# Kernel tuning notes

Measured on AMD Instinct MI355X. Metric: run time of the kernel, lower is better.

Reference implementation:

```python
import jax, jax.numpy as jnp
import numpy as np

B, S, D = 4, 2048, 1024
E, H = 1024, 16
HD = E // H
TEMPERATURE = 1.0


def setup_inputs() -> dict:
    key = jax.random.key(0)
    ks = jax.random.split(key, 6)
    x = jax.random.normal(ks[0], (B, S, D), dtype=jnp.float32)
    src_key_padding_mask = jnp.zeros((B, S), dtype=bool)  # unused by module
    matrix_mask = jax.random.normal(ks[1], (B, S, S), dtype=jnp.float32)
    # Xavier-uniform linear weights (torch Linear stores [out, in])
    lim_qkv = float(np.sqrt(6.0 / (D + 3 * E)))
    qkv_w = jax.random.uniform(ks[2], (3 * E, D), dtype=jnp.float32, minval=-lim_qkv, maxval=lim_qkv)
    qkv_b = jnp.zeros((3 * E,), dtype=jnp.float32)
    lim_o = float(np.sqrt(6.0 / (E + E)))
    o_w = jax.random.uniform(ks[3], (E, E), dtype=jnp.float32, minval=-lim_o, maxval=lim_o)
    o_b = jnp.zeros((E,), dtype=jnp.float32)
    return {"x": x, "src_key_padding_mask": src_key_padding_mask, "matrix_mask": matrix_mask,
            "qkv_w": qkv_w, "qkv_b": qkv_b, "o_w": o_w, "o_b": o_b}


def reference(x, src_key_padding_mask, matrix_mask, qkv_w, qkv_b, o_w, o_b):
    b, s, _ = x.shape
    qkv = x @ qkv_w.T + qkv_b                      # [B,S,3E]
    qkv = qkv.reshape(b, s, H, 3 * HD).transpose(0, 2, 1, 3)  # [B,H,S,3*HD]
    q, k, v = jnp.split(qkv, 3, axis=-1)           # each [B,H,S,HD]
    scale = 1.0 / np.sqrt(HD)
    logits = jnp.einsum('bhqd,bhkd->bhqk', q, k) * scale + matrix_mask[:, None, :, :]
    attn = jax.nn.softmax(logits / TEMPERATURE, axis=-1)  # [B,H,S,S]
    # dropout=0.0, eval mode -> no-op
    values = jnp.einsum('bhqk,bhkd->bhqd', attn, v)       # [B,H,S,HD]
    values = values.transpose(0, 2, 1, 3).reshape(b, s, E)
    o = values @ o_w.T + o_b                       # [B,S,E]
    attention_mean = jnp.mean(attn, axis=1)        # [B,S,S]
    return (o, attention_mean)
```

## Files before the change

### kernel.cpp

```cpp
#include <hip/hip_runtime.h>

#define B_ 4
#define S_ 2048
#define D_ 1024
#define E_ 1024
#define H_ 16
#define HD_ 64
#define SCALE 0.125f
#define LOG2E 1.44269504f
#define C1_ (SCALE * LOG2E)

typedef __bf16 bf16;
typedef __bf16 bf16x8 __attribute__((ext_vector_type(8)));
typedef __bf16 bf16x4 __attribute__((ext_vector_type(4)));
typedef float f32x4 __attribute__((ext_vector_type(4)));
typedef _Float16 f16x8 __attribute__((ext_vector_type(8)));
typedef _Float16 f16x4 __attribute__((ext_vector_type(4)));

static __device__ __forceinline__ f32x4 mfma16(bf16x8 a, bf16x8 b, f32x4 c) {
  return __builtin_amdgcn_mfma_f32_16x16x32_bf16(a, b, c, 0, 0, 0);
}

typedef __attribute__((address_space(3))) void lvoid;
typedef const __attribute__((address_space(1))) void gvoid;
static __device__ __forceinline__ void gload16(const void* g, void* l) {
  __builtin_amdgcn_global_load_lds((gvoid*)g, (lvoid*)l, 16, 0, 0);
}

static __device__ __forceinline__ float exp2a(float x) {
  float r;
  asm("v_exp_f32 %0, %1" : "=v"(r) : "v"(x));
  return r;
}

static __device__ __forceinline__ int rsw(int row) {
  return (row & 3) | (((row >> 3) & 1) << 2);
}

__global__ __launch_bounds__(256) void k_cvtall(const float* __restrict__ x, bf16* __restrict__ xb,
                                                const float* __restrict__ qkvw, bf16* __restrict__ wb,
                                                const float* __restrict__ ow, bf16* __restrict__ owb,
                                                const float* __restrict__ msk, _Float16* __restrict__ bm) {
  int bid = blockIdx.x;
  const float* src;
  int i;
  if (bid < 8192) {
    i = bid * 256 + threadIdx.x;
    float4 v = reinterpret_cast<const float4*>(x)[i];
    bf16x4 o = { (bf16)v.x, (bf16)v.y, (bf16)v.z, (bf16)v.w };
    reinterpret_cast<bf16x4*>(xb)[i] = o;
  } else if (bid < 11264) {
    i = (bid - 8192) * 256 + threadIdx.x;
    float4 v = reinterpret_cast<const float4*>(qkvw)[i];
    bf16x4 o = { (bf16)v.x, (bf16)v.y, (bf16)v.z, (bf16)v.w };
    reinterpret_cast<bf16x4*>(wb)[i] = o;
  } else if (bid < 12288) {
    i = (bid - 11264) * 256 + threadIdx.x;
    float4 v = reinterpret_cast<const float4*>(ow)[i];
    bf16x4 o = { (bf16)v.x, (bf16)v.y, (bf16)v.z, (bf16)v.w };
    reinterpret_cast<bf16x4*>(owb)[i] = o;
  } else {
    i = (bid - 12288) * 256 + threadIdx.x;
    float4 v = reinterpret_cast<const float4*>(msk)[i];
    f16x4 o = { (_Float16)(v.x * LOG2E), (_Float16)(v.y * LOG2E),
                (_Float16)(v.z * LOG2E), (_Float16)(v.w * LOG2E) };
    reinterpret_cast<f16x4*>(bm)[i] = o;
  }
  (void)src;
}

__global__ __launch_bounds__(256) void k_qkv(const bf16* __restrict__ xb,
                                             const bf16* __restrict__ wb,
                                             const float* __restrict__ qkvb,
                                             bf16* __restrict__ Qw,
                                             bf16* __restrict__ Kw,
                                             bf16* __restrict__ Vtw) {
  __shared__ __align__(16) bf16 lA[128 * 32];
  __shared__ __align__(16) bf16 lB[128 * 32];
  const int tid = threadIdx.x, lane = tid & 63, wv = tid >> 6;
  const int u = lane >> 4, c = lane & 15;
  const int wr = wv >> 1, wc = wv & 1;
  const int m0 = blockIdx.y * 128;
  const int n0 = blockIdx.x * 128;
  const int sr = tid >> 2, sk = (tid & 3) * 8;
  const bf16* gA = xb + (size_t)(m0 + sr) * D_ + sk;
  const bf16* gB = wb + (size_t)(n0 + sr) * D_ + sk;
  bf16* lpA = lA + wv * 512;
  bf16* lpB = lB + wv * 512;
  f32x4 acc[4][4] = {};
  for (int k0 = 0; k0 < D_; k0 += 32) {
    gload16(gA + k0, lpA);
    gload16(gA + 64 * D_ + k0, lpA + 2048);
    gload16(gB + k0, lpB);
    gload16(gB + 64 * D_ + k0, lpB + 2048);
    __syncthreads();
    bf16x8 af[4], bfr[4];
#pragma unroll
    for (int m = 0; m < 4; ++m)
      af[m] = *(const bf16x8*)(lA + (wr * 64 + m * 16 + c) * 32 + u * 8);
#pragma unroll
    for (int n = 0; n < 4; ++n)
      bfr[n] = *(const bf16x8*)(lB + (wc * 64 + n * 16 + c) * 32 + u * 8);
#pragma unroll
    for (int m = 0; m < 4; ++m)
#pragma unroll
      for (int n = 0; n < 4; ++n)
        acc[m][n] = mfma16(af[m], bfr[n], acc[m][n]);
    __syncthreads();
  }
#pragma unroll
  for (int n = 0; n < 4; ++n) {
    int nn = n0 + wc * 64 + n * 16 + c;
    float bias = qkvb[nn];
    int h = nn / 192;
    int rem = nn - h * 192;
#pragma unroll
    for (int m = 0; m < 4; ++m) {
#pragma unroll
      for (int r = 0; r < 4; ++r) {
        int q = m0 + wr * 64 + m * 16 + 4 * u + r;
        int bb = q >> 11, s = q & 2047;
        bf16 v = (bf16)(acc[m][n][r] + bias);
        if (rem < 64)       Qw[((bb * H_ + h) * S_ + s) * HD_ + rem] = v;
        else if (rem < 128) Kw[((bb * H_ + h) * S_ + s) * HD_ + (rem - 64)] = v;
        else                Vtw[((bb * H_ + h) * HD_ + (rem - 128)) * S_ + s] = v;
      }
    }
  }
}

#define PV_TILE2(HC, HN, BS, KT, PF)                                          \
  {                                                                           \
    f32x4 sA[4], sB[4];                                                       \
    _Pragma("unroll")                                                         \
    for (int f = 0; f < 4; ++f) {                                             \
      int rk = 32 * (f & 1) + 8 * (c >> 2) + 4 * (f >> 1) + (c & 3);          \
      int sw = rsw(rk);                                                       \
      bf16x8 k0 = *(const bf16x8*)&kl[BS][rk * 64 + ((u ^ sw) * 8)];          \
      bf16x8 k1 = *(const bf16x8*)&kl[BS][rk * 64 + (((4 + u) ^ sw) * 8)];    \
      f32x4 a = {};                                                           \
      a = mfma16(k0, aqA0, a);                                                \
      a = mfma16(k1, aqA1, a);                                                \
      sA[f] = a;                                                              \
      f32x4 bb2 = {};                                                         \
      bb2 = mfma16(k0, aqB0, bb2);                                            \
      bb2 = mfma16(k1, aqB1, bb2);                                            \
      sB[f] = bb2;                                                            \
    }                                                                         \
    if (PF) {                                                                 \
      const bf16* ksrc = Kb + (size_t)((KT) + 1) * 64 * HD_;                  \
      gload16(ksrc + ksw1, (bf16*)kl[(BS) ^ 1] + wv * 512);                   \
      gload16(ksrc + ksw2, (bf16*)kl[(BS) ^ 1] + 2048 + wv * 512);            \
      const bf16* vsrc = Vb + (size_t)((KT) + 1) * 64;                        \
      gload16(vsrc + vsw1, (bf16*)vl[(BS) ^ 1] + wv * 512);                   \
      gload16(vsrc + vsw2, (bf16*)vl[(BS) ^ 1] + 2048 + wv * 512);            \
      const _Float16* nA = bmrA + ((KT) + 1) * 64 + 8 * u;                    \
      const _Float16* nB = bmrB + ((KT) + 1) * 64 + 8 * u;                    \
      HN[0] = *(const f16x8*)(nA);                                            \
      HN[1] = *(const f16x8*)(nA + 32);                                       \
      HN[2] = *(const f16x8*)(nB);                                            \
      HN[3] = *(const f16x8*)(nB + 32);                                       \
    }                                                                         \
    float pA[16], pB[16];                                                     \
    _Pragma("unroll")                                                         \
    for (int f = 0; f < 4; ++f) {                                             \
      _Pragma("unroll")                                                       \
      for (int j = 0; j < 4; ++j) {                                           \
        float p = exp2a(sA[f][j] * C1_ + (float)HC[f & 1][4 * (f >> 1) + j]); \
        lsumA += p;                                                           \
        pA[f * 4 + j] = p;                                                    \
        float q2 = exp2a(sB[f][j] * C1_ +                                     \
                         (float)HC[2 + (f & 1)][4 * (f >> 1) + j]);           \
        lsumB += q2;                                                          \
        pB[f * 4 + j] = q2;                                                   \
      }                                                                       \
    }                                                                         \
    bf16x8 bpA0 = { (bf16)pA[0],  (bf16)pA[1],  (bf16)pA[2],  (bf16)pA[3],    \
                    (bf16)pA[8],  (bf16)pA[9],  (bf16)pA[10], (bf16)pA[11] }; \
    bf16x8 bpA1 = { (bf16)pA[4],  (bf16)pA[5],  (bf16)pA[6],  (bf16)pA[7],    \
                    (bf16)pA[12], (bf16)pA[13], (bf16)pA[14], (bf16)pA[15] }; \
    bf16x8 bpB0 = { (bf16)pB[0],  (bf16)pB[1],  (bf16)pB[2],  (bf16)pB[3],    \
                    (bf16)pB[8],  (bf16)pB[9],  (bf16)pB[10], (bf16)pB[11] }; \
    bf16x8 bpB1 = { (bf16)pB[4],  (bf16)pB[5],  (bf16)pB[6],  (bf16)pB[7],    \
                    (bf16)pB[12], (bf16)pB[13], (bf16)pB[14], (bf16)pB[15] }; \
    __builtin_amdgcn_s_setprio(1);                                            \
    _Pragma("unroll")                                                         \
    for (int g = 0; g < 4; ++g) {                                             \
      int rv = g * 16 + c;                                                    \
      int swv = rsw(rv);                                                      \
      bf16x8 v0 = *(const bf16x8*)&vl[BS][rv * 64 + ((u ^ swv) * 8)];         \
      bf16x8 v1 = *(const bf16x8*)&vl[BS][rv * 64 + (((4 + u) ^ swv) * 8)];   \
      accA[g] = mfma16(v0, bpA0, accA[g]);                                    \
      accA[g] = mfma16(v1, bpA1, accA[g]);                                    \
      accB[g] = mfma16(v0, bpB0, accB[g]);                                    \
      accB[g] = mfma16(v1, bpB1, accB[g]);                                    \
    }                                                                         \
    __builtin_amdgcn_s_setprio(0);                                            \
    __syncthreads();                                                          \
  }

__global__ __launch_bounds__(256) void k_pv(const bf16* __restrict__ Qw,
                                            const bf16* __restrict__ Kw,
                                            const bf16* __restrict__ Vtw,
                                            const _Float16* __restrict__ bmask,
                                            float* __restrict__ li_ws,
                                            bf16* __restrict__ valw) {
  __shared__ __align__(16) bf16 kl[2][64 * 64];
  __shared__ __align__(16) bf16 vl[2][64 * 64];
  const int tid = threadIdx.x, lane = tid & 63, wv = tid >> 6;
  const int u = lane >> 4, c = lane & 15;
  const int qt = blockIdx.x, h = blockIdx.y, b = blockIdx.z;
  const bf16* Qb = Qw + (size_t)(b * H_ + h) * S_ * HD_;
  const bf16* Kb = Kw + (size_t)(b * H_ + h) * S_ * HD_;
  const bf16* Vb = Vtw + (size_t)(b * H_ + h) * HD_ * S_;
  const int qrA = qt * 128 + wv * 32 + c;
  const int qrB = qrA + 16;
  bf16x8 aqA0 = *(const bf16x8*)(Qb + (size_t)qrA * HD_ + u * 8);
  bf16x8 aqA1 = *(const bf16x8*)(Qb + (size_t)qrA * HD_ + 32 + u * 8);
  bf16x8 aqB0 = *(const bf16x8*)(Qb + (size_t)qrB * HD_ + u * 8);
  bf16x8 aqB1 = *(const bf16x8*)(Qb + (size_t)qrB * HD_ + 32 + u * 8);
  const _Float16* bmrA = bmask + (size_t)b * S_ * S_ + (size_t)qrA * S_;
  const _Float16* bmrB = bmask + (size_t)b * S_ * S_ + (size_t)qrB * S_;
  const int r1 = tid >> 3, s1 = (tid & 7) ^ rsw(tid >> 3);
  const int g2i = tid + 256;
  const int r2 = g2i >> 3, s2 = (g2i & 7) ^ rsw(g2i >> 3);
  const int ksw1 = (r1 * 8 + s1) * 8, ksw2 = (r2 * 8 + s2) * 8;
  const int vsw1 = r1 * S_ + s1 * 8, vsw2 = r2 * S_ + s2 * 8;
  gload16(Kb + ksw1, (bf16*)kl[0] + wv * 512);
  gload16(Kb + ksw2, (bf16*)kl[0] + 2048 + wv * 512);
  gload16(Vb + vsw1, (bf16*)vl[0] + wv * 512);
  gload16(Vb + vsw2, (bf16*)vl[0] + 2048 + wv * 512);
  f16x8 hmA[4], hmB[4];
  hmA[0] = *(const f16x8*)(bmrA + 8 * u);
  hmA[1] = *(const f16x8*)(bmrA + 32 + 8 * u);
  hmA[2] = *(const f16x8*)(bmrB + 8 * u);
  hmA[3] = *(const f16x8*)(bmrB + 32 + 8 * u);
  f32x4 accA[4] = {}, accB[4] = {};
  float lsumA = 0.f, lsumB = 0.f;
  __syncthreads();
  for (int kt2 = 0; kt2 < 16; ++kt2) {
    PV_TILE2(hmA, hmB, 0, 2 * kt2, true);
    PV_TILE2(hmB, hmA, 1, 2 * kt2 + 1, (kt2 < 15));
  }
  lsumA += __shfl_xor(lsumA, 16, 64);
  lsumA += __shfl_xor(lsumA, 32, 64);
  lsumB += __shfl_xor(lsumB, 16, 64);
  lsumB += __shfl_xor(lsumB, 32, 64);
  float liA = 1.f / lsumA, liB = 1.f / lsumB;
  if (u == 0) {
    li_ws[(b * H_ + h) * S_ + qrA] = liA;
    li_ws[(b * H_ + h) * S_ + qrB] = liB;
  }
#pragma unroll
  for (int g = 0; g < 4; ++g) {
    bf16x4 pkA = { (bf16)(accA[g][0] * liA), (bf16)(accA[g][1] * liA),
                   (bf16)(accA[g][2] * liA), (bf16)(accA[g][3] * liA) };
    *(bf16x4*)(&valw[(size_t)(b * S_ + qrA) * E_ + h * HD_ + g * 16 + 4 * u]) = pkA;
    bf16x4 pkB = { (bf16)(accB[g][0] * liB), (bf16)(accB[g][1] * liB),
                   (bf16)(accB[g][2] * liB), (bf16)(accB[g][3] * liB) };
    *(bf16x4*)(&valw[(size_t)(b * S_ + qrB) * E_ + h * HD_ + g * 16 + 4 * u]) = pkB;
  }
}

#define MEAN_PHASE(QC0, QC1, QC2, QC3, QN0, QN1, QN2, QN3, BS, HH, PF)         \
  {                                                                            \
    if (PF) {                                                                  \
      const bf16* ksrc = Kw + (size_t)(bh0 + (HH) + 1) * S_ * HD_ +            \
                         (size_t)kt * 64 * HD_;                                \
      gload16(ksrc + sw1, (bf16*)kl2[(BS) ^ 1] + wv * 512);                    \
      gload16(ksrc + sw2, (bf16*)kl2[(BS) ^ 1] + 2048 + wv * 512);             \
      __builtin_amdgcn_sched_barrier(0);                                       \
    }                                                                          \
    bf16x8 kf[8];                                                              \
    _Pragma("unroll")                                                          \
    for (int f = 0; f < 4; ++f) {                                              \
      int row = f * 16 + c;                                                    \
      int sw = row & 7;                                                        \
      kf[2 * f]     = *(const bf16x8*)&kl2[BS][row * 64 + ((u ^ sw) * 8)];     \
      kf[2 * f + 1] = *(const bf16x8*)&kl2[BS][row * 64 + (((4 + u) ^ sw) * 8)];\
    }                                                                          \
    if (PF) {                                                                  \
      const bf16* Qn = Qw + (size_t)(bh0 + (HH) + 1) * S_ * HD_ +              \
                       (size_t)(qrow0 + c) * HD_ + u * 8;                      \
      QN0 = *(const bf16x8*)(Qn);                                              \
      QN1 = *(const bf16x8*)(Qn + 32);                                         \
      QN2 = *(const bf16x8*)(Qn + 64 * HD_);                                   \
      QN3 = *(const bf16x8*)(Qn + 64 * HD_ + 32);                              \
    }                                                                          \
    float llA = li_l[(HH) * 128 + wv * 16 + c];                                \
    float llB = li_l[(HH) * 128 + 64 + wv * 16 + c];                           \
    _Pragma("unroll")                                                          \
    for (int f = 0; f < 4; ++f) {                                              \
      f32x4 a = {};                                                            \
      a = mfma16(kf[2 * f], QC0, a);                                           \
      a = mfma16(kf[2 * f + 1], QC1, a);                                       \
      f32x4 bb = {};                                                           \
      bb = mfma16(kf[2 * f], QC2, bb);                                         \
      bb = mfma16(kf[2 * f + 1], QC3, bb);                                     \
      _Pragma("unroll")                                                        \
      for (int j = 0; j < 4; ++j) {                                            \
        maccA[f][j] += exp2a(a[j] * C1_ + (float)mhA[f][j]) * llA;             \
        maccB[f][j] += exp2a(bb[j] * C1_ + (float)mhB[f][j]) * llB;            \
      }                                                                        \
    }                                                                          \
    asm volatile("s_waitcnt vmcnt(4) lgkmcnt(0)" ::: "memory");                \
    __builtin_amdgcn_s_barrier();                                              \
  }

__global__ __launch_bounds__(256) void k_mean(const bf16* __restrict__ Qw,
                                              const bf16* __restrict__ Kw,
                                              const _Float16* __restrict__ bmask,
                                              const float* __restrict__ li_ws,
                                              float* __restrict__ mean_out) {
  __shared__ float li_l[H_ * 128];
  __shared__ __align__(16) bf16 kl2[2][64 * 64];
  const int tid = threadIdx.x, lane = tid & 63, wv = tid >> 6;
  const int u = lane >> 4, c = lane & 15;
  const int qt = blockIdx.x, kt = blockIdx.y, b = blockIdx.z;
  const int bh0 = b * H_;
  for (int i = tid; i < H_ * 128; i += 256) {
    int hh = i >> 7, q = i & 127;
    li_l[i] = li_ws[(bh0 + hh) * S_ + qt * 128 + q];
  }
  const int qrow0 = qt * 128 + wv * 16;
  f16x4 mhA[4], mhB[4];
  {
    const _Float16* bmpA = bmask + (size_t)b * S_ * S_ +
                           (size_t)(qrow0 + c) * S_ + (size_t)kt * 64 + 4 * u;
    const _Float16* bmpB = bmpA + (size_t)64 * S_;
#pragma unroll
    for (int f = 0; f < 4; ++f) {
      mhA[f] = *(const f16x4*)(bmpA + f * 16);
      mhB[f] = *(const f16x4*)(bmpB + f * 16);
    }
  }
  const int gg1 = wv * 64 + lane;
  const int gg2 = gg1 + 256;
  const int sw1 = (gg1 ^ ((gg1 >> 3) & 7)) * 8;
  const int sw2 = (gg2 ^ ((gg2 >> 3) & 7)) * 8;
  {
    const bf16* K0 = Kw + (size_t)bh0 * S_ * HD_ + (size_t)kt * 64 * HD_;
    gload16(K0 + sw1, (bf16*)kl2[0] + wv * 512);
    gload16(K0 + sw2, (bf16*)kl2[0] + 2048 + wv * 512);
  }
  bf16x8 qA0, qA1, qA2, qA3, qB0, qB1, qB2, qB3;
  {
    const bf16* Q0 = Qw + (size_t)bh0 * S_ * HD_ + (size_t)(qrow0 + c) * HD_ + u * 8;
    qA0 = *(const bf16x8*)Q0;
    qA1 = *(const bf16x8*)(Q0 + 32);
    qA2 = *(const bf16x8*)(Q0 + 64 * HD_);
    qA3 = *(const bf16x8*)(Q0 + 64 * HD_ + 32);
  }
  f32x4 maccA[4] = {}, maccB[4] = {};
  __syncthreads();
  for (int h2 = 0; h2 < 8; ++h2) {
    MEAN_PHASE(qA0, qA1, qA2, qA3, qB0, qB1, qB2, qB3, 0, 2 * h2, true);
    MEAN_PHASE(qB0, qB1, qB2, qB3, qA0, qA1, qA2, qA3, 1, 2 * h2 + 1, (h2 < 7));
  }
#pragma unroll
  for (int f = 0; f < 4; ++f) {
    f32x4 moA = maccA[f] * (1.f / 16.f);
    *(f32x4*)&mean_out[(size_t)b * S_ * S_ + (size_t)(qrow0 + c) * S_ +
                       (size_t)kt * 64 + f * 16 + 4 * u] = moA;
    f32x4 moB = maccB[f] * (1.f / 16.f);
    *(f32x4*)&mean_out[(size_t)b * S_ * S_ + (size_t)(qrow0 + 64 + c) * S_ +
                       (size_t)kt * 64 + f * 16 + 4 * u] = moB;
  }
}

__global__ __launch_bounds__(256) void k_oproj(const bf16* __restrict__ vb,
                                               const bf16* __restrict__ wo,
                                               const float* __restrict__ ob,
                                               float* __restrict__ out) {
  __shared__ __align__(16) bf16 lA[128 * 32];
  __shared__ __align__(16) bf16 lB[128 * 32];
  const int tid = threadIdx.x, lane = tid & 63, wv = tid >> 6;
  const int u = lane >> 4, c = lane & 15;
  const int wr = wv >> 1, wc = wv & 1;
  const int m0 = blockIdx.y * 128;
  const int n0 = blockIdx.x * 128;
  const int sr = tid >> 2, sk = (tid & 3) * 8;
  const bf16* gA = vb + (size_t)(m0 + sr) * E_ + sk;
  const bf16* gB = wo + (size_t)(n0 + sr) * E_ + sk;
  bf16* lpA = lA + wv * 512;
  bf16* lpB = lB + wv * 512;
  f32x4 acc[4][4] = {};
  for (int k0 = 0; k0 < E_; k0 += 32) {
    gload16(gA + k0, lpA);
    gload16(gA + 64 * E_ + k0, lpA + 2048);
    gload16(gB + k0, lpB);
    gload16(gB + 64 * E_ + k0, lpB + 2048);
    __syncthreads();
    bf16x8 af[4], bfr[4];
#pragma unroll
    for (int m = 0; m < 4; ++m)
      af[m] = *(const bf16x8*)(lA + (wr * 64 + m * 16 + c) * 32 + u * 8);
#pragma unroll
    for (int n = 0; n < 4; ++n)
      bfr[n] = *(const bf16x8*)(lB + (wc * 64 + n * 16 + c) * 32 + u * 8);
#pragma unroll
    for (int m = 0; m < 4; ++m)
#pragma unroll
      for (int n = 0; n < 4; ++n)
        acc[m][n] = mfma16(af[m], bfr[n], acc[m][n]);
    __syncthreads();
  }
#pragma unroll
  for (int n = 0; n < 4; ++n) {
    int nn = n0 + wc * 64 + n * 16 + c;
    float bias = ob[nn];
#pragma unroll
    for (int m = 0; m < 4; ++m) {
#pragma unroll
      for (int r = 0; r < 4; ++r) {
        int q = m0 + wr * 64 + m * 16 + 4 * u + r;
        out[(size_t)q * E_ + nn] = acc[m][n][r] + bias;
      }
    }
  }
}

extern "C" void kernel_launch(void* const* d_in, const int* in_sizes, int n_in,
                              void* d_out, int out_size, void* d_ws, size_t ws_size,
                              hipStream_t stream) {
  const float* x    = (const float*)d_in[0];
  const float* mmsk = (const float*)d_in[2];
  const float* qkvw = (const float*)d_in[3];
  const float* qkvb = (const float*)d_in[4];
  const float* ow   = (const float*)d_in[5];
  const float* ob   = (const float*)d_in[6];

  char* ws = (char*)d_ws;
  bf16* xb  = (bf16*)(ws);
  bf16* wb  = (bf16*)(ws + (16u << 20));
  bf16* owb = (bf16*)(ws + (22u << 20));
  bf16* Qw  = (bf16*)(ws + (24u << 20));
  bf16* Kw  = (bf16*)(ws + (40u << 20));
  bf16* Vtw = (bf16*)(ws + (56u << 20));
  float* li_ws = (float*)(ws + (16u << 20));
  bf16* values = xb;

  float* out_o    = (float*)d_out;
  float* out_mean = out_o + (size_t)B_ * S_ * E_;
  _Float16* bmask = (_Float16*)out_o;

  k_cvtall<<<dim3(28672), 256, 0, stream>>>(x, xb, qkvw, wb, ow, owb, mmsk, bmask);
  k_qkv<<<dim3(24, 64), 256, 0, stream>>>(xb, wb, qkvb, Qw, Kw, Vtw);
  k_pv<<<dim3(16, 16, 4), 256, 0, stream>>>(Qw, Kw, Vtw, bmask, li_ws, values);
  k_mean<<<dim3(16, 32, 4), 256, 0, stream>>>(Qw, Kw, bmask, li_ws, out_mean);
  k_oproj<<<dim3(8, 64), 256, 0, stream>>>(values, owb, ob, out_o);
}
```

Before: 331.1 us.

## Merge attention-mean and output-projection kernels into one horizontally fused launch

Combines the k_mean and k_oproj kernels into a single launch of 2560 blocks: the first 2048 compute the head-averaged attention map and the remaining 512 do the output projection GEMM, sharing one 24KB shared-memory buffer. The bf16-scaled mask moves from the output buffer into workspace, because the projection now writes out_o while mean blocks may still read the mask. This removes one launch boundary and lets the GEMM tail overlap the mean work. The cost is that occupancy is bounded by the larger shared-memory and register footprint of the two paths.

```diff
diff --git a/kernel.cpp b/kernel.cpp
--- a/kernel.cpp
+++ b/kernel.cpp
@@ -42,7 +42,6 @@
                                                 const float* __restrict__ ow, bf16* __restrict__ owb,
                                                 const float* __restrict__ msk, _Float16* __restrict__ bm) {
   int bid = blockIdx.x;
-  const float* src;
   int i;
   if (bid < 8192) {
     i = bid * 256 + threadIdx.x;
@@ -66,7 +65,6 @@
                 (_Float16)(v.z * LOG2E), (_Float16)(v.w * LOG2E) };
     reinterpret_cast<f16x4*>(bm)[i] = o;
   }
-  (void)src;
 }
 
 __global__ __launch_bounds__(256) void k_qkv(const bf16* __restrict__ xb,
@@ -267,8 +265,8 @@
     if (PF) {                                                                  \
       const bf16* ksrc = Kw + (size_t)(bh0 + (HH) + 1) * S_ * HD_ +            \
                          (size_t)kt * 64 * HD_;                                \
-      gload16(ksrc + sw1, (bf16*)kl2[(BS) ^ 1] + wv * 512);                    \
-      gload16(ksrc + sw2, (bf16*)kl2[(BS) ^ 1] + 2048 + wv * 512);             \
+      gload16(ksrc + sw1, (bf16*)(kl2 + ((BS) ^ 1) * 4096) + wv * 512);        \
+      gload16(ksrc + sw2, (bf16*)(kl2 + ((BS) ^ 1) * 4096) + 2048 + wv * 512); \
       __builtin_amdgcn_sched_barrier(0);                                       \
     }                                                                          \
     bf16x8 kf[8];                                                              \
@@ -276,8 +274,8 @@
     for (int f = 0; f < 4; ++f) {                                              \
       int row = f * 16 + c;                                                    \
       int sw = row & 7;                                                        \
-      kf[2 * f]     = *(const bf16x8*)&kl2[BS][row * 64 + ((u ^ sw) * 8)];     \
-      kf[2 * f + 1] = *(const bf16x8*)&kl2[BS][row * 64 + (((4 + u) ^ sw) * 8)];\
+      kf[2 * f]     = *(const bf16x8*)&kl2[(BS) * 4096 + row * 64 + ((u ^ sw) * 8)]; \
+      kf[2 * f + 1] = *(const bf16x8*)&kl2[(BS) * 4096 + row * 64 + (((4 + u) ^ sw) * 8)]; \
     }                                                                          \
     if (PF) {                                                                  \
       const bf16* Qn = Qw + (size_t)(bh0 + (HH) + 1) * S_ * HD_ +              \
@@ -307,114 +305,116 @@
     __builtin_amdgcn_s_barrier();                                              \
   }
 
-__global__ __launch_bounds__(256) void k_mean(const bf16* __restrict__ Qw,
-                                              const bf16* __restrict__ Kw,
-                                              const _Float16* __restrict__ bmask,
-                                              const float* __restrict__ li_ws,
-                                              float* __restrict__ mean_out) {
-  __shared__ float li_l[H_ * 128];
-  __shared__ __align__(16) bf16 kl2[2][64 * 64];
+__global__ __launch_bounds__(256) void k_mo(const bf16* __restrict__ Qw,
+                                            const bf16* __restrict__ Kw,
+                                            const _Float16* __restrict__ bmask,
+                                            const float* __restrict__ li_ws,
+                                            float* __restrict__ mean_out,
+                                            const bf16* __restrict__ vb,
+                                            const bf16* __restrict__ wo,
+                                            const float* __restrict__ ob,
+                                            float* __restrict__ out) {
+  __shared__ __align__(16) char smem[24 * 1024];
   const int tid = threadIdx.x, lane = tid & 63, wv = tid >> 6;
   const int u = lane >> 4, c = lane & 15;
-  const int qt = blockIdx.x, kt = blockIdx.y, b = blockIdx.z;
-  const int bh0 = b * H_;
-  for (int i = tid; i < H_ * 128; i += 256) {
-    int hh = i >> 7, q = i & 127;
-    li_l[i] = li_ws[(bh0 + hh) * S_ + qt * 128 + q];
-  }
-  const int qrow0 = qt * 128 + wv * 16;
-  f16x4 mhA[4], mhB[4];
-  {
-    const _Float16* bmpA = bmask + (size_t)b * S_ * S_ +
-                           (size_t)(qrow0 + c) * S_ + (size_t)kt * 64 + 4 * u;
-    const _Float16* bmpB = bmpA + (size_t)64 * S_;
+  const int bid = blockIdx.x;
+  if (bid < 2048) {
+    float* li_l = (float*)smem;
+    bf16* kl2 = (bf16*)(smem + 8192);
+    const int qt = bid & 15, kt = (bid >> 4) & 31, b = bid >> 9;
+    const int bh0 = b * H_;
+    for (int i = tid; i < H_ * 128; i += 256) {
+      int hh = i >> 7, q = i & 127;
+      li_l[i] = li_ws[(bh0 + hh) * S_ + qt * 128 + q];
+    }
+    const int qrow0 = qt * 128 + wv * 16;
+    f16x4 mhA[4], mhB[4];
+    {
+      const _Float16* bmpA = bmask + (size_t)b * S_ * S_ +
+                             (size_t)(qrow0 + c) * S_ + (size_t)kt * 64 + 4 * u;
+      const _Float16* bmpB = bmpA + (size_t)64 * S_;
+#pragma unroll
+      for (int f = 0; f < 4; ++f) {
+        mhA[f] = *(const f16x4*)(bmpA + f * 16);
+        mhB[f] = *(const f16x4*)(bmpB + f * 16);
+      }
+    }
+    const int gg1 = wv * 64 + lane;
+    const int gg2 = gg1 + 256;
+    const int sw1 = (gg1 ^ ((gg1 >> 3) & 7)) * 8;
+    const int sw2 = (gg2 ^ ((gg2 >> 3) & 7)) * 8;
+    {
+      const bf16* K0 = Kw + (size_t)bh0 * S_ * HD_ + (size_t)kt * 64 * HD_;
+      gload16(K0 + sw1, kl2 + wv * 512);
+      gload16(K0 + sw2, kl2 + 2048 + wv * 512);
+    }
+    bf16x8 qA0, qA1, qA2, qA3, qB0, qB1, qB2, qB3;
+    {
+      const bf16* Q0 = Qw + (size_t)bh0 * S_ * HD_ + (size_t)(qrow0 + c) * HD_ + u * 8;
+      qA0 = *(const bf16x8*)Q0;
+      qA1 = *(const bf16x8*)(Q0 + 32);
+      qA2 = *(const bf16x8*)(Q0 + 64 * HD_);
+      qA3 = *(const bf16x8*)(Q0 + 64 * HD_ + 32);
+    }
+    f32x4 maccA[4] = {}, maccB[4] = {};
+    __syncthreads();
+    for (int h2 = 0; h2 < 8; ++h2) {
+      MEAN_PHASE(qA0, qA1, qA2, qA3, qB0, qB1, qB2, qB3, 0, 2 * h2, true);
+      MEAN_PHASE(qB0, qB1, qB2, qB3, qA0, qA1, qA2, qA3, 1, 2 * h2 + 1, (h2 < 7));
+    }
 #pragma unroll
     for (int f = 0; f < 4; ++f) {
-      mhA[f] = *(const f16x4*)(bmpA + f * 16);
-      mhB[f] = *(const f16x4*)(bmpB + f * 16);
-    }
-  }
-  const int gg1 = wv * 64 + lane;
-  const int gg2 = gg1 + 256;
-  const int sw1 = (gg1 ^ ((gg1 >> 3) & 7)) * 8;
-  const int sw2 = (gg2 ^ ((gg2 >> 3) & 7)) * 8;
-  {
-    const bf16* K0 = Kw + (size_t)bh0 * S_ * HD_ + (size_t)kt * 64 * HD_;
-    gload16(K0 + sw1, (bf16*)kl2[0] + wv * 512);
-    gload16(K0 + sw2, (bf16*)kl2[0] + 2048 + wv * 512);
-  }
-  bf16x8 qA0, qA1, qA2, qA3, qB0, qB1, qB2, qB3;
-  {
-    const bf16* Q0 = Qw + (size_t)bh0 * S_ * HD_ + (size_t)(qrow0 + c) * HD_ + u * 8;
-    qA0 = *(const bf16x8*)Q0;
-    qA1 = *(const bf16x8*)(Q0 + 32);
-    qA2 = *(const bf16x8*)(Q0 + 64 * HD_);
-    qA3 = *(const bf16x8*)(Q0 + 64 * HD_ + 32);
-  }
-  f32x4 maccA[4] = {}, maccB[4] = {};
-  __syncthreads();
-  for (int h2 = 0; h2 < 8; ++h2) {
-    MEAN_PHASE(qA0, qA1, qA2, qA3, qB0, qB1, qB2, qB3, 0, 2 * h2, true);
-    MEAN_PHASE(qB0, qB1, qB2, qB3, qA0, qA1, qA2, qA3, 1, 2 * h2 + 1, (h2 < 7));
-  }
-#pragma unroll
-  for (int f = 0; f < 4; ++f) {
-    f32x4 moA = maccA[f] * (1.f / 16.f);
-    *(f32x4*)&mean_out[(size_t)b * S_ * S_ + (size_t)(qrow0 + c) * S_ +
-                       (size_t)kt * 64 + f * 16 + 4 * u] = moA;
-    f32x4 moB = maccB[f] * (1.f / 16.f);
-    *(f32x4*)&mean_out[(size_t)b * S_ * S_ + (size_t)(qrow0 + 64 + c) * S_ +
-                       (size_t)kt * 64 + f * 16 + 4 * u] = moB;
-  }
-}
-
-__global__ __launch_bounds__(256) void k_oproj(const bf16* __restrict__ vb,
-                                               const bf16* __restrict__ wo,
-                                               const float* __restrict__ ob,
-                                               float* __restrict__ out) {
-  __shared__ __align__(16) bf16 lA[128 * 32];
-  __shared__ __align__(16) bf16 lB[128 * 32];
-  const int tid = threadIdx.x, lane = tid & 63, wv = tid >> 6;
-  const int u = lane >> 4, c = lane & 15;
-  const int wr = wv >> 1, wc = wv & 1;
-  const int m0 = blockIdx.y * 128;
-  const int n0 = blockIdx.x * 128;
-  const int sr = tid >> 2, sk = (tid & 3) * 8;
-  const bf16* gA = vb + (size_t)(m0 + sr) * E_ + sk;
-  const bf16* gB = wo + (size_t)(n0 + sr) * E_ + sk;
-  bf16* lpA = lA + wv * 512;
-  bf16* lpB = lB + wv * 512;
-  f32x4 acc[4][4] = {};
-  for (int k0 = 0; k0 < E_; k0 += 32) {
-    gload16(gA + k0, lpA);
-    gload16(gA + 64 * E_ + k0, lpA + 2048);
-    gload16(gB + k0, lpB);
-    gload16(gB + 64 * E_ + k0, lpB + 2048);
-    __syncthreads();
-    bf16x8 af[4], bfr[4];
-#pragma unroll
-    for (int m = 0; m < 4; ++m)
-      af[m] = *(const bf16x8*)(lA + (wr * 64 + m * 16 + c) * 32 + u * 8);
-#pragma unroll
-    for (int n = 0; n < 4; ++n)
-      bfr[n] = *(const bf16x8*)(lB + (wc * 64 + n * 16 + c) * 32 + u * 8);
-#pragma unroll
-    for (int m = 0; m < 4; ++m)
+      f32x4 moA = maccA[f] * (1.f / 16.f);
+      *(f32x4*)&mean_out[(size_t)b * S_ * S_ + (size_t)(qrow0 + c) * S_ +
+                         (size_t)kt * 64 + f * 16 + 4 * u] = moA;
+      f32x4 moB = maccB[f] * (1.f / 16.f);
+      *(f32x4*)&mean_out[(size_t)b * S_ * S_ + (size_t)(qrow0 + 64 + c) * S_ +
+                         (size_t)kt * 64 + f * 16 + 4 * u] = moB;
+    }
+  } else {
+    bf16* lA = (bf16*)smem;
+    bf16* lB = (bf16*)(smem + 8192);
+    const int bid2 = bid - 2048;
+    const int wr = wv >> 1, wc = wv & 1;
+    const int m0 = (bid2 >> 3) * 128;
+    const int n0 = (bid2 & 7) * 128;
+    const int sr = tid >> 2, sk = (tid & 3) * 8;
+    const bf16* gA = vb + (size_t)(m0 + sr) * E_ + sk;
+    const bf16* gB = wo + (size_t)(n0 + sr) * E_ + sk;
+    bf16* lpA = lA + wv * 512;
+    bf16* lpB = lB + wv * 512;
+    f32x4 acc[4][4] = {};
+    for (int k0 = 0; k0 < E_; k0 += 32) {
+      gload16(gA + k0, lpA);
+      gload16(gA + 64 * E_ + k0, lpA + 2048);
+      gload16(gB + k0, lpB);
+      gload16(gB + 64 * E_ + k0, lpB + 2048);
+      __syncthreads();
+      bf16x8 af[4], bfr[4];
+#pragma unroll
+      for (int m = 0; m < 4; ++m)
+        af[m] = *(const bf16x8*)(lA + (wr * 64 + m * 16 + c) * 32 + u * 8);
 #pragma unroll
       for (int n = 0; n < 4; ++n)
-        acc[m][n] = mfma16(af[m], bfr[n], acc[m][n]);
-    __syncthreads();
-  }
-#pragma unroll
-  for (int n = 0; n < 4; ++n) {
-    int nn = n0 + wc * 64 + n * 16 + c;
-    float bias = ob[nn];
-#pragma unroll
-    for (int m = 0; m < 4; ++m) {
-#pragma unroll
-      for (int r = 0; r < 4; ++r) {
-        int q = m0 + wr * 64 + m * 16 + 4 * u + r;
-        out[(size_t)q * E_ + nn] = acc[m][n][r] + bias;
+        bfr[n] = *(const bf16x8*)(lB + (wc * 64 + n * 16 + c) * 32 + u * 8);
+#pragma unroll
+      for (int m = 0; m < 4; ++m)
+#pragma unroll
+        for (int n = 0; n < 4; ++n)
+          acc[m][n] = mfma16(af[m], bfr[n], acc[m][n]);
+      __syncthreads();
+    }
+#pragma unroll
+    for (int n = 0; n < 4; ++n) {
+      int nn = n0 + wc * 64 + n * 16 + c;
+      float bias = ob[nn];
+#pragma unroll
+      for (int m = 0; m < 4; ++m) {
+#pragma unroll
+        for (int r = 0; r < 4; ++r) {
+          int q = m0 + wr * 64 + m * 16 + 4 * u + r;
+          out[(size_t)q * E_ + nn] = acc[m][n][r] + bias;
+        }
       }
     }
   }
@@ -442,11 +442,11 @@
 
   float* out_o    = (float*)d_out;
   float* out_mean = out_o + (size_t)B_ * S_ * E_;
-  _Float16* bmask = (_Float16*)out_o;
+  _Float16* bmask = (_Float16*)(ws + (72u << 20));
 
   k_cvtall<<<dim3(28672), 256, 0, stream>>>(x, xb, qkvw, wb, ow, owb, mmsk, bmask);
   k_qkv<<<dim3(24, 64), 256, 0, stream>>>(xb, wb, qkvb, Qw, Kw, Vtw);
   k_pv<<<dim3(16, 16, 4), 256, 0, stream>>>(Qw, Kw, Vtw, bmask, li_ws, values);
-  k_mean<<<dim3(16, 32, 4), 256, 0, stream>>>(Qw, Kw, bmask, li_ws, out_mean);
-  k_oproj<<<dim3(8, 64), 256, 0, stream>>>(values, owb, ob, out_o);
-}
+  k_mo<<<dim3(2560), 256, 0, stream>>>(Qw, Kw, bmask, li_ws, out_mean,
+                                       values, owb, ob, out_o);
+}
```

Result: no change. 332.3 us (+0.4%).

## Split mean kernel into single-wave blocks without barriers and prefetch row inverses

Applied to the files above, without the earlier changes.

The attention-mean kernel now launches one 64-thread wave per block. Each wave loads its own 64x64 K tile into LDS with eight async loads and uses only waitcnt, so the block-wide barriers between head phases are gone. The LDS staging of per-row inverse sums is replaced by register prefetch that alternates between heads. The biased mask buffer moves from the output region into workspace. In exchange, each wave now reloads the K tile the four waves used to share, which multiplies K traffic, and the grid grows to 8192 blocks.

```diff
diff --git a/kernel.cpp b/kernel.cpp
--- a/kernel.cpp
+++ b/kernel.cpp
@@ -42,7 +42,6 @@
                                                 const float* __restrict__ ow, bf16* __restrict__ owb,
                                                 const float* __restrict__ msk, _Float16* __restrict__ bm) {
   int bid = blockIdx.x;
-  const float* src;
   int i;
   if (bid < 8192) {
     i = bid * 256 + threadIdx.x;
@@ -66,7 +65,6 @@
                 (_Float16)(v.z * LOG2E), (_Float16)(v.w * LOG2E) };
     reinterpret_cast<f16x4*>(bm)[i] = o;
   }
-  (void)src;
 }
 
 __global__ __launch_bounds__(256) void k_qkv(const bf16* __restrict__ xb,
@@ -262,13 +260,13 @@
   }
 }
 
-#define MEAN_PHASE(QC0, QC1, QC2, QC3, QN0, QN1, QN2, QN3, BS, HH, PF)         \
+#define MEAN_PH(QC0, QC1, QC2, QC3, QN0, QN1, QN2, QN3, LCA, LCB, LNA, LNB, BS, HH, PF) \
   {                                                                            \
     if (PF) {                                                                  \
-      const bf16* ksrc = Kw + (size_t)(bh0 + (HH) + 1) * S_ * HD_ +            \
-                         (size_t)kt * 64 * HD_;                                \
-      gload16(ksrc + sw1, (bf16*)kl2[(BS) ^ 1] + wv * 512);                    \
-      gload16(ksrc + sw2, (bf16*)kl2[(BS) ^ 1] + 2048 + wv * 512);             \
+      const bf16* ksrc = Kb0 + (size_t)((HH) + 1) * S_ * HD_;                  \
+      _Pragma("unroll")                                                        \
+      for (int g = 0; g < 8; ++g)                                              \
+        gload16(ksrc + koff[g], (bf16*)kl2[(BS) ^ 1] + g * 512);               \
       __builtin_amdgcn_sched_barrier(0);                                       \
     }                                                                          \
     bf16x8 kf[8];                                                              \
@@ -280,15 +278,15 @@
       kf[2 * f + 1] = *(const bf16x8*)&kl2[BS][row * 64 + (((4 + u) ^ sw) * 8)];\
     }                                                                          \
     if (PF) {                                                                  \
-      const bf16* Qn = Qw + (size_t)(bh0 + (HH) + 1) * S_ * HD_ +              \
-                       (size_t)(qrow0 + c) * HD_ + u * 8;                      \
+      const bf16* Qn = Qb0 + (size_t)((HH) + 1) * S_ * HD_;                    \
       QN0 = *(const bf16x8*)(Qn);                                              \
       QN1 = *(const bf16x8*)(Qn + 32);                                         \
       QN2 = *(const bf16x8*)(Qn + 64 * HD_);                                   \
       QN3 = *(const bf16x8*)(Qn + 64 * HD_ + 32);                              \
+      const float* lp = lb0 + (size_t)((HH) + 1) * S_;                         \
+      LNA = lp[0];                                                             \
+      LNB = lp[64];                                                            \
     }                                                                          \
-    float llA = li_l[(HH) * 128 + wv * 16 + c];                                \
-    float llB = li_l[(HH) * 128 + 64 + wv * 16 + c];                           \
     _Pragma("unroll")                                                          \
     for (int f = 0; f < 4; ++f) {                                              \
       f32x4 a = {};                                                            \
@@ -299,30 +297,25 @@
       bb = mfma16(kf[2 * f + 1], QC3, bb);                                     \
       _Pragma("unroll")                                                        \
       for (int j = 0; j < 4; ++j) {                                            \
-        maccA[f][j] += exp2a(a[j] * C1_ + (float)mhA[f][j]) * llA;             \
-        maccB[f][j] += exp2a(bb[j] * C1_ + (float)mhB[f][j]) * llB;            \
+        maccA[f][j] += exp2a(a[j] * C1_ + (float)mhA[f][j]) * LCA;             \
+        maccB[f][j] += exp2a(bb[j] * C1_ + (float)mhB[f][j]) * LCB;            \
       }                                                                        \
     }                                                                          \
-    asm volatile("s_waitcnt vmcnt(4) lgkmcnt(0)" ::: "memory");                \
-    __builtin_amdgcn_s_barrier();                                              \
-  }
-
-__global__ __launch_bounds__(256) void k_mean(const bf16* __restrict__ Qw,
-                                              const bf16* __restrict__ Kw,
-                                              const _Float16* __restrict__ bmask,
-                                              const float* __restrict__ li_ws,
-                                              float* __restrict__ mean_out) {
-  __shared__ float li_l[H_ * 128];
+    if (PF) asm volatile("s_waitcnt vmcnt(6) lgkmcnt(0)" ::: "memory");        \
+  }
+
+__global__ __launch_bounds__(64) void k_mean(const bf16* __restrict__ Qw,
+                                             const bf16* __restrict__ Kw,
+                                             const _Float16* __restrict__ bmask,
+                                             const float* __restrict__ li_ws,
+                                             float* __restrict__ mean_out) {
   __shared__ __align__(16) bf16 kl2[2][64 * 64];
-  const int tid = threadIdx.x, lane = tid & 63, wv = tid >> 6;
+  const int lane = threadIdx.x;
   const int u = lane >> 4, c = lane & 15;
-  const int qt = blockIdx.x, kt = blockIdx.y, b = blockIdx.z;
+  const int bid = blockIdx.x;
+  const int ws = bid & 3, qt = (bid >> 2) & 15, kt = (bid >> 6) & 31, b = bid >> 11;
   const int bh0 = b * H_;
-  for (int i = tid; i < H_ * 128; i += 256) {
-    int hh = i >> 7, q = i & 127;
-    li_l[i] = li_ws[(bh0 + hh) * S_ + qt * 128 + q];
-  }
-  const int qrow0 = qt * 128 + wv * 16;
+  const int qrow0 = qt * 128 + ws * 16;
   f16x4 mhA[4], mhB[4];
   {
     const _Float16* bmpA = bmask + (size_t)b * S_ * S_ +
@@ -334,28 +327,32 @@
       mhB[f] = *(const f16x4*)(bmpB + f * 16);
     }
   }
-  const int gg1 = wv * 64 + lane;
-  const int gg2 = gg1 + 256;
-  const int sw1 = (gg1 ^ ((gg1 >> 3) & 7)) * 8;
-  const int sw2 = (gg2 ^ ((gg2 >> 3) & 7)) * 8;
-  {
-    const bf16* K0 = Kw + (size_t)bh0 * S_ * HD_ + (size_t)kt * 64 * HD_;
-    gload16(K0 + sw1, (bf16*)kl2[0] + wv * 512);
-    gload16(K0 + sw2, (bf16*)kl2[0] + 2048 + wv * 512);
-  }
+  int koff[8];
+#pragma unroll
+  for (int g = 0; g < 8; ++g) {
+    int gg = g * 64 + lane;
+    int r = gg >> 3, s = (gg & 7) ^ (r & 7);
+    koff[g] = (r * 8 + s) * 8;
+  }
+  const bf16* Kb0 = Kw + (size_t)bh0 * S_ * HD_ + (size_t)kt * 64 * HD_;
+  const bf16* Qb0 = Qw + (size_t)bh0 * S_ * HD_ + (size_t)(qrow0 + c) * HD_ + u * 8;
+  const float* lb0 = li_ws + (size_t)bh0 * S_ + qrow0 + c;
+#pragma unroll
+  for (int g = 0; g < 8; ++g)
+    gload16(Kb0 + koff[g], (bf16*)kl2[0] + g * 512);
+  __builtin_amdgcn_sched_barrier(0);
   bf16x8 qA0, qA1, qA2, qA3, qB0, qB1, qB2, qB3;
-  {
-    const bf16* Q0 = Qw + (size_t)bh0 * S_ * HD_ + (size_t)(qrow0 + c) * HD_ + u * 8;
-    qA0 = *(const bf16x8*)Q0;
-    qA1 = *(const bf16x8*)(Q0 + 32);
-    qA2 = *(const bf16x8*)(Q0 + 64 * HD_);
-    qA3 = *(const bf16x8*)(Q0 + 64 * HD_ + 32);
-  }
+  qA0 = *(const bf16x8*)(Qb0);
+  qA1 = *(const bf16x8*)(Qb0 + 32);
+  qA2 = *(const bf16x8*)(Qb0 + 64 * HD_);
+  qA3 = *(const bf16x8*)(Qb0 + 64 * HD_ + 32);
+  float lcA = lb0[0], lcB = lb0[64];
+  float lnA, lnB;
   f32x4 maccA[4] = {}, maccB[4] = {};
-  __syncthreads();
+  asm volatile("s_waitcnt vmcnt(6) lgkmcnt(0)" ::: "memory");
   for (int h2 = 0; h2 < 8; ++h2) {
-    MEAN_PHASE(qA0, qA1, qA2, qA3, qB0, qB1, qB2, qB3, 0, 2 * h2, true);
-    MEAN_PHASE(qB0, qB1, qB2, qB3, qA0, qA1, qA2, qA3, 1, 2 * h2 + 1, (h2 < 7));
+    MEAN_PH(qA0, qA1, qA2, qA3, qB0, qB1, qB2, qB3, lcA, lcB, lnA, lnB, 0, 2 * h2, true);
+    MEAN_PH(qB0, qB1, qB2, qB3, qA0, qA1, qA2, qA3, lnA, lnB, lcA, lcB, 1, 2 * h2 + 1, (h2 < 7));
   }
 #pragma unroll
   for (int f = 0; f < 4; ++f) {
@@ -439,14 +436,14 @@
   bf16* Vtw = (bf16*)(ws + (56u << 20));
   float* li_ws = (float*)(ws + (16u << 20));
   bf16* values = xb;
+  _Float16* bmask = (_Float16*)(ws + (72u << 20));
 
   float* out_o    = (float*)d_out;
   float* out_mean = out_o + (size_t)B_ * S_ * E_;
-  _Float16* bmask = (_Float16*)out_o;
 
   k_cvtall<<<dim3(28672), 256, 0, stream>>>(x, xb, qkvw, wb, ow, owb, mmsk, bmask);
   k_qkv<<<dim3(24, 64), 256, 0, stream>>>(xb, wb, qkvb, Qw, Kw, Vtw);
   k_pv<<<dim3(16, 16, 4), 256, 0, stream>>>(Qw, Kw, Vtw, bmask, li_ws, values);
-  k_mean<<<dim3(16, 32, 4), 256, 0, stream>>>(Qw, Kw, bmask, li_ws, out_mean);
+  k_mean<<<dim3(8192), 64, 0, stream>>>(Qw, Kw, bmask, li_ws, out_mean);
   k_oproj<<<dim3(8, 64), 256, 0, stream>>>(values, owb, ob, out_o);
 }
```

Result: slower. 343.6 us (+3.8%).
